# Optimization experiments

Hardware: AMD Instinct MI355X
Metric: run time of the kernel (lower is better)

## Reference

```python
import jax, jax.numpy as jnp
import numpy as np

B, T, WIN, HID = 256, 16384, 5, 5  # hidden must equal window for mse_loss shapes to match


def setup_inputs() -> dict:
    key = jax.random.key(0)
    k1, k2, k3 = jax.random.split(key, 3)
    series = jax.random.normal(k1, (B, T), dtype=jnp.float32)
    # nn.Linear(window_size, hidden_size) params: weight [H, W], bias [H]
    bound = 1.0 / np.sqrt(WIN)
    weight = jax.random.uniform(k2, (HID, WIN), jnp.float32, -bound, bound)
    bias = jax.random.uniform(k3, (HID,), jnp.float32, -bound, bound)
    threshold = jnp.float32(0.1)  # change_point_threshold parameter
    return {"series": series, "weight": weight, "bias": bias, "threshold": threshold}


def reference(series, weight, bias, threshold):
    Bb, Tt = series.shape
    H, Wd = weight.shape
    N = Tt - Wd  # number of windows = time_steps - window_size
    # Gather all sliding windows at once: idx [N, W]
    idx = jnp.arange(N)[:, None] + jnp.arange(Wd)[None, :]
    local = series[:, idx]        # [B, N, W]  == series[:, i:i+W] for all i
    target = series[:, idx + 1]   # [B, N, W]  == series[:, i+1:i+W+1]
    # Tiny per-window linear, batched over all windows
    transformed = jnp.einsum('bnw,hw->bnh', local, weight) + bias  # [B, N, H]
    # F.mse_loss reduces over all elements (B and H) per window
    losses = jnp.mean((transformed - target) ** 2, axis=(0, 2))    # [N]
    # change-point logic vectorized: diff of consecutive losses vs threshold
    diffs = jnp.abs(losses[1:] - losses[:-1])                      # [N-1]
    change_mask = diffs > threshold                                # [N-1] bool
    return losses, diffs, change_mask
```

## Files before the change

kernel.cpp:

```cpp
#include <hip/hip_runtime.h>

#define BB    256
#define TT    16384
#define WIN   5
#define HID   5
#define NN    (TT - WIN)
#define TILE  32
#define NT    512
#define NCOLS (TILE + WIN + 1)
#define LDSW  44

__global__ __launch_bounds__(256)
void llsa_fused(const float* __restrict__ series,
                const float* __restrict__ weight,
                const float* __restrict__ bias,
                const float* __restrict__ thr_ptr,
                float* __restrict__ out) {
    const int tid = threadIdx.x;
    const int t  = (blockIdx.x & 7) * 64 + (blockIdx.x >> 3);
    const int n0 = t * TILE;

    float w[HID][WIN], bi[HID];
#pragma unroll
    for (int h = 0; h < HID; ++h) {
        bi[h] = bias[h];
#pragma unroll
        for (int v = 0; v < WIN; ++v) w[h][v] = weight[h * WIN + v];
    }

    __shared__ float lds[BB * LDSW];
    __shared__ float psum[8 * TILE];
    __shared__ float Ls[TILE + 1];

    {
        const int c4 = (tid & 7) * 4;
        const int rb = tid >> 3;
#pragma unroll
        for (int it = 0; it < 8; ++it) {
            const int r = it * 32 + rb;
            const float4 v = *(const float4*)(series + (size_t)r * TT + n0 + c4);
            *(float4*)(&lds[r * LDSW + c4]) = v;
        }
    }
    {
        const float* row = series + (size_t)tid * TT;
#pragma unroll
        for (int j = 0; j < WIN + 1; ++j) {
            const int col = n0 + TILE + j;
            lds[tid * LDSW + TILE + j] = (col < TT) ? row[col] : 0.f;
        }
    }
    __syncthreads();

    const int c    = tid & (TILE - 1);
    const int rsub = tid >> 5;
    float ax = 0.f, ay = 0.f;
#pragma unroll
    for (int k = 0; k < 32; k += 2) {
        const float* rA = &lds[(rsub * 32 + k) * LDSW + c];
        const float* rB = rA + LDSW;
        float sx[WIN + 1], sy[WIN + 1];
#pragma unroll
        for (int j = 0; j <= WIN; ++j) { sx[j] = rA[j]; sy[j] = rB[j]; }
#pragma unroll
        for (int h = 0; h < HID; ++h) {
            float tx = bi[h], ty = bi[h];
#pragma unroll
            for (int v = 0; v < WIN; ++v) {
                tx = fmaf(sx[v], w[h][v], tx);
                ty = fmaf(sy[v], w[h][v], ty);
            }
            const float ex = tx - sx[h + 1];
            const float ey = ty - sy[h + 1];
            ax = fmaf(ex, ex, ax);
            ay = fmaf(ey, ey, ay);
        }
    }
    const float acc = ax + ay;

    float bacc = 0.f;
    if (tid < 64) {
#pragma unroll
        for (int s = 0; s < 4; ++s) {
            const float* row = &lds[(tid + 64 * s) * LDSW + TILE];
            float sv[WIN + 1];
#pragma unroll
            for (int j = 0; j <= WIN; ++j) sv[j] = row[j];
#pragma unroll
            for (int h = 0; h < HID; ++h) {
                float tt = bi[h];
#pragma unroll
                for (int v = 0; v < WIN; ++v) tt = fmaf(sv[v], w[h][v], tt);
                const float e = tt - sv[h + 1];
                bacc = fmaf(e, e, bacc);
            }
        }
    }
    float bs = bacc;
#pragma unroll
    for (int off = 32; off >= 1; off >>= 1) bs += __shfl_down(bs, off);

    psum[rsub * TILE + c] = acc;
    __syncthreads();

    const float inv = 1.0f / (float)(BB * HID);
    if (tid == 0) Ls[TILE] = bs * inv;
    if (tid < TILE) {
        float s = 0.f;
#pragma unroll
        for (int g = 0; g < 8; ++g) s += psum[g * TILE + tid];
        Ls[tid] = s * inv;
    }
    __syncthreads();

    if (tid < TILE) {
        const int i = n0 + tid;
        if (i < NN) {
            const float li = Ls[tid];
            out[i] = li;
            if (i < NN - 1) {
                const float d = fabsf(Ls[tid + 1] - li);
                out[NN + i] = d;
                out[2 * NN - 1 + i] = (d > thr_ptr[0]) ? 1.0f : 0.0f;
            }
        }
    }
}

extern "C" void kernel_launch(void* const* d_in, const int* in_sizes, int n_in,
                              void* d_out, int out_size, void* d_ws, size_t ws_size,
                              hipStream_t stream) {
    const float* series = (const float*)d_in[0];
    const float* weight = (const float*)d_in[1];
    const float* bias   = (const float*)d_in[2];
    const float* thr    = (const float*)d_in[3];
    float* out = (float*)d_out;
    (void)d_ws; (void)ws_size; (void)in_sizes; (void)n_in; (void)out_size;

    llsa_fused<<<NT, 256, 0, stream>>>(series, weight, bias, thr, out);
}
```

Before: 75.24 us.

## Vectorize LDS reads with per-thread 4-window register sliding and float4 halo loads

Measured after the change: 73.10 us. 1.03x faster.

```diff
diff --git a/kernel.cpp b/kernel.cpp
--- a/kernel.cpp
+++ b/kernel.cpp
@@ -7,7 +7,6 @@
 #define NN    (TT - WIN)
 #define TILE  32
 #define NT    512
-#define NCOLS (TILE + WIN + 1)
 #define LDSW  44
 
 __global__ __launch_bounds__(256)
@@ -29,7 +28,7 @@
     }
 
     __shared__ float lds[BB * LDSW];
-    __shared__ float psum[8 * TILE];
+    __shared__ float psum[32 * 33];
     __shared__ float Ls[TILE + 1];
 
     {
@@ -43,46 +42,54 @@
         }
     }
     {
-        const float* row = series + (size_t)tid * TT;
 #pragma unroll
-        for (int j = 0; j < WIN + 1; ++j) {
-            const int col = n0 + TILE + j;
-            lds[tid * LDSW + TILE + j] = (col < TT) ? row[col] : 0.f;
+        for (int it = 0; it < 2; ++it) {
+            const int idx = it * 256 + tid;
+            const int r   = idx >> 1;
+            const int cc  = 32 + (idx & 1) * 4;
+            const int col = n0 + cc;
+            float4 v = make_float4(0.f, 0.f, 0.f, 0.f);
+            if (col + 3 < TT) {
+                v = *(const float4*)(series + (size_t)r * TT + col);
+            }
+            *(float4*)(&lds[r * LDSW + cc]) = v;
         }
     }
     __syncthreads();
 
-    const int c    = tid & (TILE - 1);
-    const int rsub = tid >> 5;
-    float ax = 0.f, ay = 0.f;
+    const int cq = tid & 7;
+    const int rs = tid >> 3;
+    float a0 = 0.f, a1 = 0.f, a2 = 0.f, a3 = 0.f;
 #pragma unroll
-    for (int k = 0; k < 32; k += 2) {
-        const float* rA = &lds[(rsub * 32 + k) * LDSW + c];
-        const float* rB = rA + LDSW;
-        float sx[WIN + 1], sy[WIN + 1];
+    for (int k = 0; k < 8; ++k) {
+        const float* row = &lds[(rs * 8 + k) * LDSW + 4 * cq];
+        const float4 f0 = *(const float4*)(row);
+        const float4 f1 = *(const float4*)(row + 4);
+        const float4 f2 = *(const float4*)(row + 8);
+        const float s[12] = { f0.x, f0.y, f0.z, f0.w,
+                              f1.x, f1.y, f1.z, f1.w,
+                              f2.x, f2.y, f2.z, f2.w };
 #pragma unroll
-        for (int j = 0; j <= WIN; ++j) { sx[j] = rA[j]; sy[j] = rB[j]; }
+        for (int j = 0; j < 4; ++j) {
+            float aj = 0.f;
 #pragma unroll
-        for (int h = 0; h < HID; ++h) {
-            float tx = bi[h], ty = bi[h];
+            for (int h = 0; h < HID; ++h) {
+                float tt = bi[h];
 #pragma unroll
-            for (int v = 0; v < WIN; ++v) {
-                tx = fmaf(sx[v], w[h][v], tx);
-                ty = fmaf(sy[v], w[h][v], ty);
+                for (int v = 0; v < WIN; ++v) tt = fmaf(s[j + v], w[h][v], tt);
+                const float e = tt - s[j + h + 1];
+                aj = fmaf(e, e, aj);
             }
-            const float ex = tx - sx[h + 1];
-            const float ey = ty - sy[h + 1];
-            ax = fmaf(ex, ex, ax);
-            ay = fmaf(ey, ey, ay);
+            if (j == 0) a0 += aj; else if (j == 1) a1 += aj;
+            else if (j == 2) a2 += aj; else a3 += aj;
         }
     }
-    const float acc = ax + ay;
 
     float bacc = 0.f;
     if (tid < 64) {
 #pragma unroll
-        for (int s = 0; s < 4; ++s) {
-            const float* row = &lds[(tid + 64 * s) * LDSW + TILE];
+        for (int sIt = 0; sIt < 4; ++sIt) {
+            const float* row = &lds[(tid + 64 * sIt) * LDSW + TILE];
             float sv[WIN + 1];
 #pragma unroll
             for (int j = 0; j <= WIN; ++j) sv[j] = row[j];
@@ -100,15 +107,18 @@
 #pragma unroll
     for (int off = 32; off >= 1; off >>= 1) bs += __shfl_down(bs, off);
 
-    psum[rsub * TILE + c] = acc;
+    psum[rs * 33 + 4 * cq + 0] = a0;
+    psum[rs * 33 + 4 * cq + 1] = a1;
+    psum[rs * 33 + 4 * cq + 2] = a2;
+    psum[rs * 33 + 4 * cq + 3] = a3;
+    const float inv = 1.0f / (float)(BB * HID);
+    if (tid == 0) Ls[TILE] = bs * inv;
     __syncthreads();
 
-    const float inv = 1.0f / (float)(BB * HID);
-    if (tid == 0) Ls[TILE] = bs * inv;
     if (tid < TILE) {
         float s = 0.f;
 #pragma unroll
-        for (int g = 0; g < 8; ++g) s += psum[g * TILE + tid];
+        for (int r = 0; r < 32; ++r) s += psum[r * 33 + tid];
         Ls[tid] = s * inv;
     }
     __syncthreads();
```
